# Optimization experiments

Hardware: AMD Instinct MI355X
Metric: run time of the kernel (lower is better)

Reference implementation:

```python
import jax, jax.numpy as jnp
import numpy as np

B, L, IN, DM, DS, DC, EXP = 4, 1024, 256, 1024, 16, 4, 2
DI = EXP * DM            # d_inner = 2048
DTR = (DM + 15) // 16    # dt_rank = 64


def setup_inputs() -> dict:
    key = jax.random.key(0)
    ks = jax.random.split(key, 10)
    s = lambda k, sh, sc: jax.random.normal(k, sh, jnp.float32) * sc
    return {
        "x": s(ks[0], (B, L, IN), 1.0),
        "W_emb": s(ks[1], (DM, IN), IN ** -0.5),
        "b_emb": jnp.zeros((DM,), jnp.float32),
        "in_proj_w": s(ks[2], (2 * DI, DM), DM ** -0.5),
        "conv_w": s(ks[3], (DI, 1, DC), DC ** -0.5),
        "conv_b": jnp.zeros((DI,), jnp.float32),
        "x_proj_w": s(ks[4], (DTR + 2 * DS, DI), DI ** -0.5),
        "dt_proj_w": s(ks[5], (DI, DTR), DTR ** -0.5),
        "dt_proj_b": s(ks[6], (DI,), 0.1),
        "A_log": jnp.tile(jnp.log(jnp.arange(1, DS + 1, dtype=jnp.float32)), (DI, 1)),
        "D": jnp.ones((DI,), jnp.float32),
        "out_proj_w": s(ks[7], (DM, DI), DI ** -0.5),
        "fc_w": s(ks[8], (1, DM), DM ** -0.5),
        "fc_b": jnp.zeros((1,), jnp.float32),
    }


def _forward(x, W_emb, b_emb, in_proj_w, conv_w, conv_b, x_proj_w,
             dt_proj_w, dt_proj_b, A_log, D, out_proj_w, fc_w, fc_b):
    h = x @ W_emb.T + b_emb                      # [B,L,DM] input embedding
    xz = h @ in_proj_w.T                         # [B,L,2*DI]
    u, z = jnp.split(xz, 2, axis=-1)             # each [B,L,DI]
    # causal depthwise conv over time (pad left d_conv-1)
    uc = jax.lax.conv_general_dilated(
        u.transpose(0, 2, 1), conv_w, (1,), [(DC - 1, 0)],
        dimension_numbers=('NCH', 'OIH', 'NCH'), feature_group_count=DI)
    u = jax.nn.silu(uc.transpose(0, 2, 1) + conv_b)   # [B,L,DI]
    xdbl = u @ x_proj_w.T                        # [B,L,DTR+2*DS]
    dt, Bm, Cm = jnp.split(xdbl, [DTR, DTR + DS], axis=-1)
    delta = jax.nn.softplus(dt @ dt_proj_w.T + dt_proj_b)  # [B,L,DI]
    A = -jnp.exp(A_log)                          # [DI,DS]

    def step(hst, ins):
        d_t, B_t, C_t, u_t = ins                 # [B,DI],[B,DS],[B,DS],[B,DI]
        dA = jnp.exp(d_t[..., None] * A)         # [B,DI,DS]
        hst = dA * hst + (d_t * u_t)[..., None] * B_t[:, None, :]
        y = jnp.einsum('bds,bs->bd', hst, C_t)
        return hst, y

    h0 = jnp.zeros((B, DI, DS), u.dtype)
    _, ys = jax.lax.scan(step, h0, (delta.transpose(1, 0, 2),
                                    Bm.transpose(1, 0, 2),
                                    Cm.transpose(1, 0, 2),
                                    u.transpose(1, 0, 2)))
    y = ys.transpose(1, 0, 2) + D * u            # [B,L,DI] with D skip
    y = y * jax.nn.silu(z)                       # gate
    out = y @ out_proj_w.T                       # [B,L,DM]
    return out[:, -1, :] @ fc_w.T + fc_b         # [B,1]


def reference(x, W_emb, b_emb, in_proj_w, conv_w, conv_b, x_proj_w,
              dt_proj_w, dt_proj_b, A_log, D, out_proj_w, fc_w, fc_b):
    return _forward(x, W_emb, b_emb, in_proj_w, conv_w, conv_b, x_proj_w,
                    dt_proj_w, dt_proj_b, A_log, D, out_proj_w, fc_w, fc_b)
```

## Files before the change

### kernel.cpp

```cpp
#include <hip/hip_runtime.h>
#include <cstddef>
#include <cstdint>

namespace {

typedef _Float16 half8 __attribute__((ext_vector_type(8)));
typedef _Float16 half4 __attribute__((ext_vector_type(4)));
typedef float f32x4 __attribute__((ext_vector_type(4)));

constexpr int Bn   = 4;
constexpr int Ln   = 1024;
constexpr int INn  = 256;
constexpr int DMn  = 1024;
constexpr int DSn  = 16;
constexpr int DCn  = 4;
constexpr int DIn  = 2048;
constexpr int DTRn = 64;
constexpr int XPW  = DTRn + DSn;
constexpr int NCHUNK = 64;
constexpr int CHUNK  = Ln / NCHUNK;
constexpr int WCH  = 32;
constexpr int ML   = Bn * Ln;

__device__ __forceinline__ float silu_(float x) { return x / (1.f + __expf(-x)); }
__device__ __forceinline__ float softplus_(float x) {
    return fmaxf(x, 0.f) + __logf(1.f + __expf(-fabsf(x)));
}

__global__ __launch_bounds__(256)
void prep_mega(const float* __restrict__ x, _Float16* __restrict__ xh,
               const float* __restrict__ ip, _Float16* __restrict__ iph,
               const float* __restrict__ dtw, _Float16* __restrict__ dtwh,
               const float* __restrict__ W_emb, _Float16* __restrict__ W_embT,
               const float* __restrict__ x_proj, _Float16* __restrict__ xp_h,
               const float* __restrict__ fc_w, const float* __restrict__ out_w,
               float* __restrict__ wp,
               const float* __restrict__ b_emb, float* __restrict__ badd,
               const float* __restrict__ fc_b, float* __restrict__ out) {
    __shared__ float tile[32][33];
    const int bid = blockIdx.x, tid = threadIdx.x;
    if (bid < 4096) {
        const int n = bid;
        const float4 v = ((const float4*)ip)[n * 256 + tid];
        ((half4*)iph)[n * 256 + tid] =
            half4{(_Float16)v.x, (_Float16)v.y, (_Float16)v.z, (_Float16)v.w};
        const float4 bv = ((const float4*)b_emb)[tid];
        float s = v.x * bv.x + v.y * bv.y + v.z * bv.z + v.w * bv.w;
        for (int off = 32; off > 0; off >>= 1) s += __shfl_down(s, off);
        if ((tid & 63) == 0) tile[0][tid >> 6] = s;
        __syncthreads();
        if (tid == 0) badd[n] = tile[0][0] + tile[0][1] + tile[0][2] + tile[0][3];
    } else if (bid < 5248) {
        const float* in; _Float16* outp; int i;
        if (bid < 5120) { in = x;   outp = xh;   i = (bid - 4096) * 256 + tid; }
        else            { in = dtw; outp = dtwh; i = (bid - 5120) * 256 + tid; }
        const float4 v = ((const float4*)in)[i];
        ((half4*)outp)[i] = half4{(_Float16)v.x, (_Float16)v.y, (_Float16)v.z, (_Float16)v.w};
    } else if (bid < 5504) {
        const int bx = bid - 5248;
        const int m0 = (bx & 31) * 32, c0 = (bx >> 5) * 32;
        const int lc = tid & 31, lr = tid >> 5;
        #pragma unroll
        for (int ph = 0; ph < 4; ++ph)
            tile[lr + ph * 8][lc] = W_emb[(size_t)(m0 + lr + ph * 8) * INn + c0 + lc];
        __syncthreads();
        #pragma unroll
        for (int ph = 0; ph < 4; ++ph)
            W_embT[(size_t)(c0 + lr + ph * 8) * DMn + m0 + lc] = (_Float16)tile[lc][lr + ph * 8];
    } else if (bid < 5760) {
        const int i = (bid - 5504) * 256 + tid;
        const int r = i >> 9;
        const int c4 = i & 511;
        half4 h;
        if (r < XPW) {
            const float4 v = ((const float4*)(x_proj + (size_t)r * DIn))[c4];
            h = half4{(_Float16)v.x, (_Float16)v.y, (_Float16)v.z, (_Float16)v.w};
        } else {
            h = half4{(_Float16)0.f, (_Float16)0.f, (_Float16)0.f, (_Float16)0.f};
        }
        ((half4*)(xp_h + (size_t)r * DIn))[c4] = h;
    } else if (bid < 6016) {
        const int bx = bid - 5760;
        const int d = (bx & 7) * 256 + tid;
        const int c = bx >> 3;
        const int mstep = DMn / WCH;
        float s = 0.f;
        for (int m = c * mstep; m < (c + 1) * mstep; ++m)
            s += fc_w[m] * out_w[(size_t)m * DIn + d];
        wp[(size_t)c * DIn + d] = s;
    } else {
        if (tid < Bn) out[tid] = fc_b[0];
    }
}

__global__ __launch_bounds__(256)
void skgemm2(const _Float16* __restrict__ A, int lda,
             const _Float16* __restrict__ Bw, int ldb,
             float* __restrict__ P, int N, int Kc) {
    __shared__ _Float16 As[128 * 32];
    __shared__ _Float16 Bs[128 * 32];
    const int tid  = threadIdx.x;
    const int lane = tid & 63, wid = tid >> 6;
    const int wm = wid >> 1, wn = wid & 1;
    const int sk = blockIdx.x;
    const int m0 = blockIdx.y * 128;
    const int n0 = blockIdx.z * 128;
    const int M  = gridDim.y * 128;

    f32x4 acc[4][4] = {};
    const int kbeg = sk * Kc;
    for (int k0 = kbeg; k0 < kbeg + Kc; k0 += 32) {
        #pragma unroll
        for (int i = 0; i < 2; ++i) {
            const int off = tid * 16 + i * 4096;
            const int row = off >> 6;
            const int ch  = (off & 63) >> 1;
            __builtin_amdgcn_global_load_lds(
                (const __attribute__((address_space(1))) void*)(A + (size_t)(m0 + row) * lda + k0 + ch),
                (__attribute__((address_space(3))) void*)(&As[off >> 1]), 16, 0, 0);
            __builtin_amdgcn_global_load_lds(
                (const __attribute__((address_space(1))) void*)(Bw + (size_t)(n0 + row) * ldb + k0 + ch),
                (__attribute__((address_space(3))) void*)(&Bs[off >> 1]), 16, 0, 0);
        }
        __syncthreads();
        const int ar = lane & 15;
        const int kq = (lane >> 4) * 8;
        half8 af[4], bf[4];
        #pragma unroll
        for (int i = 0; i < 4; ++i)
            af[i] = *(const half8*)&As[(wm * 64 + i * 16 + ar) * 32 + kq];
        #pragma unroll
        for (int j = 0; j < 4; ++j)
            bf[j] = *(const half8*)&Bs[(wn * 64 + j * 16 + ar) * 32 + kq];
        #pragma unroll
        for (int i = 0; i < 4; ++i)
            #pragma unroll
            for (int j = 0; j < 4; ++j)
                acc[i][j] = __builtin_amdgcn_mfma_f32_16x16x32_f16(af[i], bf[j], acc[i][j], 0, 0, 0);
        __syncthreads();
    }
    const int cr = (lane >> 4) * 4;
    const int cn = lane & 15;
    #pragma unroll
    for (int i = 0; i < 4; ++i)
        #pragma unroll
        for (int j = 0; j < 4; ++j) {
            const int n = n0 + wn * 64 + j * 16 + cn;
            if (n < N) {
                #pragma unroll
                for (int r = 0; r < 4; ++r) {
                    const int m = m0 + wm * 64 + i * 16 + cr + r;
                    P[((size_t)sk * M + m) * N + n] = acc[i][j][r];
                }
            }
        }
}

__global__ __launch_bounds__(256)
void skcomb(const float* __restrict__ P, _Float16* __restrict__ out, int total, int nsk) {
    const int i = blockIdx.x * 256 + threadIdx.x;
    if (i >= total) return;
    float s = 0.f;
    for (int k = 0; k < nsk; ++k) s += P[(size_t)k * total + i];
    out[i] = (_Float16)s;
}

__global__ __launch_bounds__(256)
void skcombB_clast(const float* __restrict__ P, _Float16* __restrict__ dtBh,
                   const _Float16* __restrict__ u, const float* __restrict__ x_proj,
                   float* __restrict__ Clast) {
    const int bid = blockIdx.x, tid = threadIdx.x;
    if (bid < 1280) {
        const int i = bid * 256 + tid;
        float s = 0.f;
        #pragma unroll
        for (int k = 0; k < 8; ++k) s += P[(size_t)k * (ML * XPW) + i];
        dtBh[i] = (_Float16)s;
    } else {
        const int wave = tid >> 6, lane = tid & 63;
        const int task = (bid - 1280) * 4 + wave;
        const int s_idx = task & 15, b = task >> 4;
        const _Float16* ur = u + ((size_t)b * Ln + (Ln - 1)) * DIn;
        const float* w = x_proj + (size_t)(XPW + s_idx) * DIn;
        float s = 0.f;
        for (int k = lane; k < DIn; k += 64) s += (float)ur[k] * w[k];
        for (int off = 32; off > 0; off >>= 1) s += __shfl_down(s, off);
        if (lane == 0) Clast[b * DSn + s_idx] = s;
    }
}

__global__ __launch_bounds__(256)
void upre_conv_zlast(const _Float16* __restrict__ xh, const _Float16* __restrict__ Wfoldh,
                     const float* __restrict__ badd,
                     const float* __restrict__ cw, const float* __restrict__ cb,
                     _Float16* __restrict__ uh,
                     const float* __restrict__ x, float* __restrict__ zlast) {
    const int tid = threadIdx.x;
    if (blockIdx.x == 16) {
        const int t = blockIdx.y * 256 + tid;
        const int j = t & (DIn - 1), b = t >> 11;
        const float4* x4 = (const float4*)(x + ((size_t)b * Ln + (Ln - 1)) * INn);
        const half4* w4 = (const half4*)(Wfoldh + (size_t)(DIn + j) * INn);
        float s = 0.f;
        #pragma unroll 8
        for (int q = 0; q < 64; ++q) {
            const float4 xv = x4[q];
            const half4 wv = w4[q];
            s += (float)wv[0] * xv.x + (float)wv[1] * xv.y
               + (float)wv[2] * xv.z + (float)wv[3] * xv.w;
        }
        zlast[(size_t)b * DIn + j] = s + badd[DIn + j];
        return;
    }
    __shared__ _Float16 smem[144 * 132];
    _Float16* As = smem;
    _Float16* Bs = smem + 144 * 32;
    _Float16 (*Ds)[132] = (_Float16 (*)[132])smem;

    const int lane = tid & 63, wid = tid >> 6;
    const int wm = wid >> 1, wn = wid & 1;
    const int m0 = blockIdx.y * 128, n0 = blockIdx.x * 128;

    f32x4 acc[4][4] = {};
    f32x4 acch[4] = {};
    for (int k0 = 0; k0 < INn; k0 += 32) {
        #pragma unroll
        for (int i = 0; i < 2; ++i) {
            const int off = tid * 16 + i * 4096;
            const int row = off >> 6;
            const int ch  = (off & 63) >> 1;
            int srow = m0 - 16 + row;
            if (srow < 0) srow = 0;
            __builtin_amdgcn_global_load_lds(
                (const __attribute__((address_space(1))) void*)(xh + (size_t)srow * INn + k0 + ch),
                (__attribute__((address_space(3))) void*)(&As[off >> 1]), 16, 0, 0);
            const _Float16* gb = Wfoldh + (size_t)(n0 + row) * INn + k0 + ch;
            __builtin_amdgcn_global_load_lds(
                (const __attribute__((address_space(1))) void*)gb,
                (__attribute__((address_space(3))) void*)(&Bs[off >> 1]), 16, 0, 0);
        }
        if (tid < 64) {
            const int off = tid * 16 + 8192;
            const int row = off >> 6;
            const int ch  = (off & 63) >> 1;
            __builtin_amdgcn_global_load_lds(
                (const __attribute__((address_space(1))) void*)(xh + (size_t)(m0 - 16 + row) * INn + k0 + ch),
                (__attribute__((address_space(3))) void*)(&As[off >> 1]), 16, 0, 0);
        }
        __syncthreads();
        const int ar = lane & 15;
        const int kq = (lane >> 4) * 8;
        half8 af[4], bf[4];
        #pragma unroll
        for (int i = 0; i < 4; ++i)
            af[i] = *(const half8*)&As[(16 + wm * 64 + i * 16 + ar) * 32 + kq];
        #pragma unroll
        for (int j = 0; j < 4; ++j)
            bf[j] = *(const half8*)&Bs[(wn * 64 + j * 16 + ar) * 32 + kq];
        #pragma unroll
        for (int i = 0; i < 4; ++i)
            #pragma unroll
            for (int j = 0; j < 4; ++j)
                acc[i][j] = __builtin_amdgcn_mfma_f32_16x16x32_f16(af[i], bf[j], acc[i][j], 0, 0, 0);
        if (wm == 0) {
            const half8 afh = *(const half8*)&As[ar * 32 + kq];
            #pragma unroll
            for (int j = 0; j < 4; ++j)
                acch[j] = __builtin_amdgcn_mfma_f32_16x16x32_f16(afh, bf[j], acch[j], 0, 0, 0);
        }
        __syncthreads();
    }

    {
        const int cr = (lane >> 4) * 4;
        const int cn = lane & 15;
        #pragma unroll
        for (int i = 0; i < 4; ++i)
            #pragma unroll
            for (int j = 0; j < 4; ++j) {
                const int col = wn * 64 + j * 16 + cn;
                const float bb = badd[n0 + col];
                #pragma unroll
                for (int r = 0; r < 4; ++r)
                    Ds[16 + wm * 64 + i * 16 + cr + r][col] = (_Float16)(acc[i][j][r] + bb);
            }
        if (wm == 0) {
            #pragma unroll
            for (int j = 0; j < 4; ++j) {
                const int col = wn * 64 + j * 16 + cn;
                const float bb = badd[n0 + col];
                #pragma unroll
                for (int r = 0; r < 4; ++r)
                    Ds[cr + r][col] = (_Float16)(acch[j][r] + bb);
            }
        }
    }
    __syncthreads();

    const int col8 = tid & 15;
    const int d0l = col8 * 8;
    f32x4 cwq[8];
    float cbv[8];
    #pragma unroll
    for (int q = 0; q < 8; ++q) {
        cwq[q] = *(const f32x4*)(cw + (size_t)(n0 + d0l + q) * DCn);
        cbv[q] = cb[n0 + d0l + q];
    }
    const int b  = m0 >> 10;
    const int t0 = m0 & 1023;
    half8 hzero;
    #pragma unroll
    for (int q = 0; q < 8; ++q) hzero[q] = (_Float16)0.f;
    for (int k = 0; k < 8; ++k) {
        const int rr = (tid >> 4) + k * 16;
        half8 w[4];
        #pragma unroll
        for (int jj = 0; jj < 4; ++jj) {
            const int dr = 16 + rr - 3 + jj;
            w[jj] = ((t0 == 0) && (dr < 16)) ? hzero : *(const half8*)&Ds[dr][d0l];
        }
        half8 o;
        #pragma unroll
        for (int q = 0; q < 8; ++q) {
            float a = cbv[q];
            #pragma unroll
            for (int jj = 0; jj < 4; ++jj) a += (float)w[jj][q] * cwq[q][jj];
            o[q] = (_Float16)silu_(a);
        }
        *(half8*)(uh + ((size_t)b * Ln + t0 + rr) * DIn + n0 + d0l) = o;
    }
}

__global__ __launch_bounds__(256)
void hgemm_delta(const _Float16* __restrict__ A, const _Float16* __restrict__ Bw,
                 const float* __restrict__ bias, _Float16* __restrict__ Ch) {
    __shared__ _Float16 As[128 * 32];
    __shared__ _Float16 Bs[128 * 32];
    const int tid  = threadIdx.x;
    const int lane = tid & 63, wid = tid >> 6;
    const int wm = wid >> 1, wn = wid & 1;
    const int m0 = blockIdx.y * 128, n0 = blockIdx.x * 128;

    f32x4 acc[4][4] = {};
    for (int k0 = 0; k0 < DTRn; k0 += 32) {
        #pragma unroll
        for (int i = 0; i < 2; ++i) {
            const int off = tid * 16 + i * 4096;
            const int row = off >> 6;
            const int ch  = (off & 63) >> 1;
            __builtin_amdgcn_global_load_lds(
                (const __attribute__((address_space(1))) void*)(A + (size_t)(m0 + row) * XPW + k0 + ch),
                (__attribute__((address_space(3))) void*)(&As[off >> 1]), 16, 0, 0);
            __builtin_amdgcn_global_load_lds(
                (const __attribute__((address_space(1))) void*)(Bw + (size_t)(n0 + row) * DTRn + k0 + ch),
                (__attribute__((address_space(3))) void*)(&Bs[off >> 1]), 16, 0, 0);
        }
        __syncthreads();
        const int ar = lane & 15;
        const int kq = (lane >> 4) * 8;
        half8 af[4], bf[4];
        #pragma unroll
        for (int i = 0; i < 4; ++i)
            af[i] = *(const half8*)&As[(wm * 64 + i * 16 + ar) * 32 + kq];
        #pragma unroll
        for (int j = 0; j < 4; ++j)
            bf[j] = *(const half8*)&Bs[(wn * 64 + j * 16 + ar) * 32 + kq];
        #pragma unroll
        for (int i = 0; i < 4; ++i)
            #pragma unroll
            for (int j = 0; j < 4; ++j)
                acc[i][j] = __builtin_amdgcn_mfma_f32_16x16x32_f16(af[i], bf[j], acc[i][j], 0, 0, 0);
        __syncthreads();
    }
    const int cr = (lane >> 4) * 4;
    const int cn = lane & 15;
    #pragma unroll
    for (int i = 0; i < 4; ++i)
        #pragma unroll
        for (int j = 0; j < 4; ++j) {
            const int n = n0 + wn * 64 + j * 16 + cn;
            #pragma unroll
            for (int r = 0; r < 4; ++r) {
                const int m = m0 + wm * 64 + i * 16 + cr + r;
                Ch[(size_t)m * DIn + n] = (_Float16)softplus_(acc[i][j][r] + bias[n]);
            }
        }
}

__global__ __launch_bounds__(256)
void scan_chunk_kernel(const _Float16* __restrict__ delta, const _Float16* __restrict__ u,
                       const _Float16* __restrict__ dtBh, const float* __restrict__ A_log,
                       float* __restrict__ cS, _Float16* __restrict__ cH) {
    const int d = blockIdx.x * 256 + threadIdx.x;
    const int c = blockIdx.y, b = blockIdx.z;
    float A[DSn], h[DSn];
    const float4* al = (const float4*)(A_log + (size_t)d * DSn);
    #pragma unroll
    for (int q = 0; q < 4; ++q) {
        const float4 v = al[q];
        A[q * 4 + 0] = -__expf(v.x); A[q * 4 + 1] = -__expf(v.y);
        A[q * 4 + 2] = -__expf(v.z); A[q * 4 + 3] = -__expf(v.w);
        h[q * 4 + 0] = 0.f; h[q * 4 + 1] = 0.f; h[q * 4 + 2] = 0.f; h[q * 4 + 3] = 0.f;
    }
    const float A0 = A[0];
    bool structured = true;
    #pragma unroll
    for (int s = 1; s < DSn; ++s)
        structured = structured && (fabsf(A[s] - (float)(s + 1) * A0) <= 1e-4f * (s + 1));
    float Ssum = 0.f;
    const size_t base = ((size_t)b * Ln + (size_t)c * CHUNK) * DIn + d;
    const _Float16* Bp = dtBh + ((size_t)b * Ln + (size_t)c * CHUNK) * XPW + DTRn;
    if (structured) {
        #pragma unroll 4
        for (int tt = 0; tt < CHUNK; ++tt) {
            const float dl = (float)delta[base + (size_t)tt * DIn];
            const float uu = (float)u[base + (size_t)tt * DIn];
            const float du = dl * uu;
            Ssum += dl;
            const half8 bv0 = *(const half8*)(Bp + tt * XPW);
            const half8 bv1 = *(const half8*)(Bp + tt * XPW + 8);
            float Bv[DSn];
            #pragma unroll
            for (int q = 0; q < 8; ++q) { Bv[q] = (float)bv0[q]; Bv[8 + q] = (float)bv1[q]; }
            const float e1 = __expf(dl * A0);
            const float e2 = e1 * e1, e4 = e2 * e2, e8 = e4 * e4;
            float E[DSn];
            E[0] = e1;      E[1] = e2;      E[2] = e2 * e1;  E[3] = e4;
            E[4] = e4 * e1; E[5] = e4 * e2; E[6] = E[5] * e1; E[7] = e8;
            E[8] = e8 * e1; E[9] = e8 * e2; E[10] = E[9] * e1; E[11] = e8 * e4;
            E[12] = E[11] * e1; E[13] = E[11] * e2; E[14] = E[13] * e1; E[15] = e8 * e8;
            #pragma unroll
            for (int s = 0; s < DSn; ++s) h[s] = E[s] * h[s] + du * Bv[s];
        }
    } else {
        #pragma unroll 4
        for (int tt = 0; tt < CHUNK; ++tt) {
            const float dl = (float)delta[base + (size_t)tt * DIn];
            const float uu = (float)u[base + (size_t)tt * DIn];
            const float du = dl * uu;
            Ssum += dl;
            const half8 bv0 = *(const half8*)(Bp + tt * XPW);
            const half8 bv1 = *(const half8*)(Bp + tt * XPW + 8);
            float Bv[DSn];
            #pragma unroll
            for (int q = 0; q < 8; ++q) { Bv[q] = (float)bv0[q]; Bv[8 + q] = (float)bv1[q]; }
            #pragma unroll
            for (int s = 0; s < DSn; ++s) h[s] = __expf(dl * A[s]) * h[s] + du * Bv[s];
        }
    }
    const size_t cidx = ((size_t)b * NCHUNK + c) * DIn + d;
    cS[cidx] = Ssum;
    half8 o0, o1;
    #pragma unroll
    for (int q = 0; q < 8; ++q) { o0[q] = (_Float16)h[q]; o1[q] = (_Float16)h[8 + q]; }
    *(half8*)(cH + cidx * DSn) = o0;
    *(half8*)(cH + cidx * DSn + 8) = o1;
}

__global__ __launch_bounds__(256)
void combine_v3(const float* __restrict__ cS, const _Float16* __restrict__ cH,
                const float* __restrict__ A_log, const float* __restrict__ Clast,
                const float* __restrict__ Dp, const _Float16* __restrict__ u,
                const float* __restrict__ zlast, const float* __restrict__ wp,
                float* __restrict__ out) {
    __shared__ float acc[16];
    const int tid = threadIdx.x;
    const int s = tid & 15;
    const int d = blockIdx.x * 16 + (tid >> 4);
    const int b = blockIdx.y;
    const float A = -__expf(A_log[(size_t)d * DSn + s]);
    float h = 0.f;
    const size_t cb0 = (size_t)b * NCHUNK;
    for (int c = 0; c < NCHUNK; ++c) {
        const size_t cidx = (cb0 + c) * DIn + d;
        h = __expf(A * cS[cidx]) * h + (float)cH[cidx * DSn + s];
    }
    float y = h * Clast[b * DSn + s];
    y += __shfl_xor(y, 1);
    y += __shfl_xor(y, 2);
    y += __shfl_xor(y, 4);
    y += __shfl_xor(y, 8);
    if (s == 0) {
        const float ul = (float)u[((size_t)b * Ln + (Ln - 1)) * DIn + d];
        float yy = y + Dp[d] * ul;
        yy *= silu_(zlast[(size_t)b * DIn + d]);
        float w = 0.f;
        #pragma unroll
        for (int c = 0; c < WCH; ++c) w += wp[(size_t)c * DIn + d];
        acc[tid >> 4] = yy * w;
    }
    __syncthreads();
    if (tid == 0) {
        float t = 0.f;
        #pragma unroll
        for (int i = 0; i < 16; ++i) t += acc[i];
        atomicAdd(&out[b], t);
    }
}

}

extern "C" void kernel_launch(void* const* d_in, const int* in_sizes, int n_in,
                              void* d_out, int out_size, void* d_ws, size_t ws_size,
                              hipStream_t stream) {
    (void)in_sizes; (void)n_in; (void)out_size; (void)ws_size;
    const float* x       = (const float*)d_in[0];
    const float* W_emb   = (const float*)d_in[1];
    const float* b_emb   = (const float*)d_in[2];
    const float* in_proj = (const float*)d_in[3];
    const float* conv_w  = (const float*)d_in[4];
    const float* conv_b  = (const float*)d_in[5];
    const float* x_proj  = (const float*)d_in[6];
    const float* dt_w    = (const float*)d_in[7];
    const float* dt_b    = (const float*)d_in[8];
    const float* A_log   = (const float*)d_in[9];
    const float* Dp      = (const float*)d_in[10];
    const float* out_w   = (const float*)d_in[11];
    const float* fc_w    = (const float*)d_in[12];
    const float* fc_b    = (const float*)d_in[13];
    float* out = (float*)d_out;
    char* w8 = (char*)d_ws;

    const size_t MB = 1ull << 20;
    _Float16* uh       = (_Float16*)(w8 + 16 * MB);
    float*    wfoldP   = (float*)(w8 + 32 * MB);
    _Float16* deltah   = (_Float16*)(w8 + 32 * MB);
    float*    skp      = (float*)(w8 + 48 * MB);
    float*    cS       = skp;
    _Float16* cH       = (_Float16*)(w8 + 50 * MB);
    _Float16* dtBh     = (_Float16*)(w8 + 67 * MB);
    _Float16* xh       = (_Float16*)(w8 + 68 * MB);
    _Float16* W_embT_h = (_Float16*)(w8 + 70 * MB);
    _Float16* in_projh = (_Float16*)(w8 + 71 * MB);
    _Float16* xp_h     = (_Float16*)(w8 + 79 * MB);
    _Float16* dt_wh    = (_Float16*)(w8 + 80 * MB);
    _Float16* Wfoldh   = (_Float16*)(w8 + 81 * MB);
    float*    wp       = (float*)(w8 + 83 * MB);
    float*    badd     = (float*)(w8 + 84 * MB);
    float*    zlast    = badd + 4096;
    float*    Clast    = zlast + (size_t)Bn * DIn;

    prep_mega<<<6017, 256, 0, stream>>>(x, xh, in_proj, in_projh, dt_w, dt_wh,
                                        W_emb, W_embT_h, x_proj, xp_h,
                                        fc_w, out_w, wp, b_emb, badd, fc_b, out);
    skgemm2<<<dim3(4, ML / 128, 2), 256, 0, stream>>>(
        in_projh, DMn, W_embT_h, DMn, wfoldP, INn, 256);
    skcomb<<<(ML * INn + 255) / 256, 256, 0, stream>>>(wfoldP, Wfoldh, ML * INn, 4);
    upre_conv_zlast<<<dim3(17, ML / 128), 256, 0, stream>>>(
        xh, Wfoldh, badd, conv_w, conv_b, uh, x, zlast);
    skgemm2<<<dim3(8, ML / 128, 1), 256, 0, stream>>>(uh, DIn, xp_h, DIn, skp, XPW, 256);
    skcombB_clast<<<1296, 256, 0, stream>>>(skp, dtBh, uh, x_proj, Clast);
    hgemm_delta<<<dim3(DIn / 128, ML / 128), 256, 0, stream>>>(dtBh, dt_wh, dt_b, deltah);
    scan_chunk_kernel<<<dim3(DIn / 256, NCHUNK, Bn), 256, 0, stream>>>(
        deltah, uh, dtBh, A_log, cS, cH);
    combine_v3<<<dim3(DIn / 16, Bn), 256, 0, stream>>>(
        cS, cH, A_log, Clast, Dp, uh, zlast, wp, out);
}
```

Baseline: 124.6 us.

## Skip z-half weight fold; compute last-step z via embedded last token

```diff
diff --git a/kernel.cpp b/kernel.cpp
--- a/kernel.cpp
+++ b/kernel.cpp
@@ -17,7 +17,7 @@
 constexpr int DIn  = 2048;
 constexpr int DTRn = 64;
 constexpr int XPW  = DTRn + DSn;
-constexpr int NCHUNK = 64;
+constexpr int NCHUNK = 32;
 constexpr int CHUNK  = Ln / NCHUNK;
 constexpr int WCH  = 32;
 constexpr int ML   = Bn * Ln;
@@ -36,7 +36,8 @@
                const float* __restrict__ fc_w, const float* __restrict__ out_w,
                float* __restrict__ wp,
                const float* __restrict__ b_emb, float* __restrict__ badd,
-               const float* __restrict__ fc_b, float* __restrict__ out) {
+               const float* __restrict__ fc_b, float* __restrict__ out,
+               float* __restrict__ e_last) {
     __shared__ float tile[32][33];
     const int bid = blockIdx.x, tid = threadIdx.x;
     if (bid < 4096) {
@@ -88,8 +89,41 @@
         for (int m = c * mstep; m < (c + 1) * mstep; ++m)
             s += fc_w[m] * out_w[(size_t)m * DIn + d];
         wp[(size_t)c * DIn + d] = s;
+    } else if (bid == 6016) {
+        if (tid < Bn) out[tid] = fc_b[0];
     } else {
-        if (tid < Bn) out[tid] = fc_b[0];
+        const int m = (bid - 6017) * 4 + (tid >> 6);
+        const int lane = tid & 63;
+        const float4 wq = ((const float4*)(W_emb + (size_t)m * INn))[lane];
+        float s0, s1, s2, s3;
+        {
+            const float4 v = ((const float4*)(x + ((size_t)0 * Ln + (Ln - 1)) * INn))[lane];
+            s0 = wq.x * v.x + wq.y * v.y + wq.z * v.z + wq.w * v.w;
+        }
+        {
+            const float4 v = ((const float4*)(x + ((size_t)1 * Ln + (Ln - 1)) * INn))[lane];
+            s1 = wq.x * v.x + wq.y * v.y + wq.z * v.z + wq.w * v.w;
+        }
+        {
+            const float4 v = ((const float4*)(x + ((size_t)2 * Ln + (Ln - 1)) * INn))[lane];
+            s2 = wq.x * v.x + wq.y * v.y + wq.z * v.z + wq.w * v.w;
+        }
+        {
+            const float4 v = ((const float4*)(x + ((size_t)3 * Ln + (Ln - 1)) * INn))[lane];
+            s3 = wq.x * v.x + wq.y * v.y + wq.z * v.z + wq.w * v.w;
+        }
+        for (int off = 32; off > 0; off >>= 1) {
+            s0 += __shfl_down(s0, off);
+            s1 += __shfl_down(s1, off);
+            s2 += __shfl_down(s2, off);
+            s3 += __shfl_down(s3, off);
+        }
+        if (lane == 0) {
+            e_last[0 * DMn + m] = s0;
+            e_last[1 * DMn + m] = s1;
+            e_last[2 * DMn + m] = s2;
+            e_last[3 * DMn + m] = s3;
+        }
     }
 }
 
@@ -194,20 +228,22 @@
                      const float* __restrict__ badd,
                      const float* __restrict__ cw, const float* __restrict__ cb,
                      _Float16* __restrict__ uh,
-                     const float* __restrict__ x, float* __restrict__ zlast) {
+                     const _Float16* __restrict__ iph, const float* __restrict__ e_last,
+                     float* __restrict__ zlast) {
     const int tid = threadIdx.x;
     if (blockIdx.x == 16) {
         const int t = blockIdx.y * 256 + tid;
-        const int j = t & (DIn - 1), b = t >> 11;
-        const float4* x4 = (const float4*)(x + ((size_t)b * Ln + (Ln - 1)) * INn);
-        const half4* w4 = (const half4*)(Wfoldh + (size_t)(DIn + j) * INn);
+        const int j = t >> 2, b = t & 3;
+        const _Float16* row = iph + (size_t)(DIn + j) * DMn;
+        const float* el = e_last + (size_t)b * DMn;
         float s = 0.f;
         #pragma unroll 8
-        for (int q = 0; q < 64; ++q) {
-            const float4 xv = x4[q];
-            const half4 wv = w4[q];
-            s += (float)wv[0] * xv.x + (float)wv[1] * xv.y
-               + (float)wv[2] * xv.z + (float)wv[3] * xv.w;
+        for (int q = 0; q < 128; ++q) {
+            const half8 w = ((const half8*)row)[q];
+            const float4 e0 = ((const float4*)el)[q * 2];
+            const float4 e1 = ((const float4*)el)[q * 2 + 1];
+            s += (float)w[0] * e0.x + (float)w[1] * e0.y + (float)w[2] * e0.z + (float)w[3] * e0.w
+               + (float)w[4] * e1.x + (float)w[5] * e1.y + (float)w[6] * e1.z + (float)w[7] * e1.w;
         }
         zlast[(size_t)b * DIn + j] = s + badd[DIn + j];
         return;
@@ -539,16 +575,17 @@
     float*    badd     = (float*)(w8 + 84 * MB);
     float*    zlast    = badd + 4096;
     float*    Clast    = zlast + (size_t)Bn * DIn;
-
-    prep_mega<<<6017, 256, 0, stream>>>(x, xh, in_proj, in_projh, dt_w, dt_wh,
+    float*    e_last   = Clast + 64;
+
+    prep_mega<<<6273, 256, 0, stream>>>(x, xh, in_proj, in_projh, dt_w, dt_wh,
                                         W_emb, W_embT_h, x_proj, xp_h,
-                                        fc_w, out_w, wp, b_emb, badd, fc_b, out);
-    skgemm2<<<dim3(4, ML / 128, 2), 256, 0, stream>>>(
+                                        fc_w, out_w, wp, b_emb, badd, fc_b, out, e_last);
+    skgemm2<<<dim3(4, 16, 2), 256, 0, stream>>>(
         in_projh, DMn, W_embT_h, DMn, wfoldP, INn, 256);
-    skcomb<<<(ML * INn + 255) / 256, 256, 0, stream>>>(wfoldP, Wfoldh, ML * INn, 4);
-    upre_conv_zlast<<<dim3(17, ML / 128), 256, 0, stream>>>(
-        xh, Wfoldh, badd, conv_w, conv_b, uh, x, zlast);
-    skgemm2<<<dim3(8, ML / 128, 1), 256, 0, stream>>>(uh, DIn, xp_h, DIn, skp, XPW, 256);
+    skcomb<<<2048, 256, 0, stream>>>(wfoldP, Wfoldh, 2048 * INn, 4);
+    upre_conv_zlast<<<dim3(17, 32), 256, 0, stream>>>(
+        xh, Wfoldh, badd, conv_w, conv_b, uh, in_projh, e_last, zlast);
+    skgemm2<<<dim3(8, 32, 1), 256, 0, stream>>>(uh, DIn, xp_h, DIn, skp, XPW, 256);
     skcombB_clast<<<1296, 256, 0, stream>>>(skp, dtBh, uh, x_proj, Clast);
     hgemm_delta<<<dim3(DIn / 128, ML / 128), 256, 0, stream>>>(dtBh, dt_wh, dt_b, deltah);
     scan_chunk_kernel<<<dim3(DIn / 256, NCHUNK, Bn), 256, 0, stream>>>(
```

Result: slower. 141.1 us (+13.2%).
